# Kernel tuning notes

Hardware: AMD Instinct MI355X
Metric: run time of the kernel (lower is better)

The kernel has to match this reference:

```python
import jax, jax.numpy as jnp
import numpy as np

D_MODEL = 768; N_LAYERS = 4; SOC_WINDOW = 10
D_INNER = 2 * D_MODEL; D_STATE = 16; DT_RANK = D_MODEL // 16; D_CONV = 4
EPS = 1e-5
B, T = 4, 1024


def setup_inputs() -> dict:
    key = jax.random.key(0)
    ks = jax.random.split(key, 10)
    w = lambda k, s, sc=0.02: jax.random.normal(k, s, jnp.float32) * sc
    return {
        "x": jax.random.normal(ks[0], (B, T, 2 + SOC_WINDOW), jnp.float32),
        "inp_w": w(ks[1], (D_MODEL, 2 + SOC_WINDOW)),
        "inp_b": jnp.zeros((D_MODEL,), jnp.float32),
        "in_proj_w": w(ks[2], (N_LAYERS, 2 * D_INNER, D_MODEL)),
        "conv_w": w(ks[3], (N_LAYERS, D_INNER, D_CONV), 0.1),
        "conv_b": jnp.zeros((N_LAYERS, D_INNER), jnp.float32),
        "x_proj_w": w(ks[4], (N_LAYERS, DT_RANK + 2 * D_STATE, D_INNER)),
        "dt_proj_w": w(ks[5], (N_LAYERS, D_INNER, DT_RANK), 0.05),
        "dt_proj_b": w(ks[6], (N_LAYERS, D_INNER), 0.5),
        "A_log": jnp.tile(jnp.log(jnp.arange(1.0, D_STATE + 1.0, dtype=jnp.float32)), (N_LAYERS, D_INNER, 1)),
        "D_skip": jnp.ones((N_LAYERS, D_INNER), jnp.float32),
        "out_proj_w": w(ks[7], (N_LAYERS, D_MODEL, D_INNER)),
        "ln_w": jnp.ones((N_LAYERS, D_MODEL), jnp.float32),
        "norm_w": jnp.ones((D_MODEL,), jnp.float32),
        "head_w": w(ks[8], (1, D_MODEL)),
        "head_b": jnp.zeros((1,), jnp.float32),
    }


def _rmsnorm(x, w):
    return x * jax.lax.rsqrt(jnp.mean(x * x, axis=-1, keepdims=True) + EPS) * w


def _mamba_block(x, in_w, cw, cb, xp_w, dtw, dtb, A_log, Dsk, out_w):
    Bsz = x.shape[0]
    xz = jnp.einsum('btd,ed->bte', x, in_w)            # (B,T,2*D_INNER)
    xx, z = jnp.split(xz, 2, axis=-1)
    # causal depthwise conv1d (pad left d_conv-1, truncate to T)
    xc = jax.lax.conv_general_dilated(
        jnp.swapaxes(xx, 1, 2), cw[:, None, :], (1,), [(D_CONV - 1, 0)],
        feature_group_count=D_INNER, dimension_numbers=('NCH', 'OIH', 'NCH'))
    xx = jax.nn.silu(jnp.swapaxes(xc + cb[None, :, None], 1, 2))  # (B,T,D_INNER)
    dbc = jnp.einsum('btd,ed->bte', xx, xp_w)          # (B,T,dt_rank+2*N)
    delta = jax.nn.softplus(jnp.einsum('btr,dr->btd', dbc[..., :DT_RANK], dtw) + dtb)
    Bm = dbc[..., DT_RANK:DT_RANK + D_STATE]           # (B,T,N)
    Cm = dbc[..., DT_RANK + D_STATE:]                  # (B,T,N)
    A = -jnp.exp(A_log)                                # (D_INNER,N)

    def step(h, inp):
        d_t, x_t, b_t, c_t = inp                       # (B,Din),(B,Din),(B,N),(B,N)
        h = jnp.exp(d_t[..., None] * A) * h + (d_t * x_t)[..., None] * b_t[:, None, :]
        return h, jnp.einsum('bdn,bn->bd', h, c_t)

    h0 = jnp.zeros((Bsz, D_INNER, D_STATE), x.dtype)
    _, ys = jax.lax.scan(step, h0, (jnp.moveaxis(delta, 1, 0), jnp.moveaxis(xx, 1, 0),
                                    jnp.moveaxis(Bm, 1, 0), jnp.moveaxis(Cm, 1, 0)))
    y = jnp.moveaxis(ys, 0, 1) + Dsk * xx
    y = y * jax.nn.silu(z)
    return jnp.einsum('bte,de->btd', y, out_w)


def reference(x, inp_w, inp_b, in_proj_w, conv_w, conv_b, x_proj_w, dt_proj_w, dt_proj_b,
              A_log, D_skip, out_proj_w, ln_w, norm_w, head_w, head_b):
    h = jnp.einsum('btf,df->btd', x, inp_w) + inp_b
    for l in range(N_LAYERS):
        h = h + _mamba_block(_rmsnorm(h, ln_w[l]), in_proj_w[l], conv_w[l], conv_b[l],
                             x_proj_w[l], dt_proj_w[l], dt_proj_b[l], A_log[l],
                             D_skip[l], out_proj_w[l])
    h = _rmsnorm(h, norm_w)
    y = jnp.einsum('btd,od->bto', h, head_w) + head_b
    return y[..., 0]
```

## Files before the change

kernel.cpp:

```cpp
#include <hip/hip_runtime.h>
#include <stdint.h>

#define D_MODEL   768
#define D_INNER   1536
#define D_STATE   16
#define DT_RANK   48
#define NB        4
#define TSEQ      1024
#define NTOK      4096
#define EPS       1e-5f
#define CHUNK     32
#define NCHUNK    32
#define XP_N      128

typedef __bf16 bf16;
typedef __bf16 bf16x8 __attribute__((ext_vector_type(8)));
typedef float  floatx4 __attribute__((ext_vector_type(4)));

__device__ __forceinline__ float silu_f(float v)     { return v / (1.f + __expf(-v)); }
__device__ __forceinline__ float softplus_f(float v) { return v > 20.f ? v : __logf(1.f + __expf(v)); }

__device__ __forceinline__ void async_ld16(const void* g, void* l) {
  __builtin_amdgcn_global_load_lds((__attribute__((address_space(1))) uint32_t*)g,
                                   (__attribute__((address_space(3))) uint32_t*)l, 16, 0, 0);
}

__global__ __launch_bounds__(256) void prep_k(const float* __restrict__ win, const float* __restrict__ wout,
                                              bf16* __restrict__ bin, bf16* __restrict__ bout) {
  const int i = blockIdx.x * 256 + threadIdx.x;
  const int NIN = 4 * 3072 * 768;
  if (i < NIN) bin[i] = (bf16)win[i];
  else         bout[i - NIN] = (bf16)wout[i - NIN];
}

__global__ __launch_bounds__(256) void prep_xp_k(const float* __restrict__ w, bf16* __restrict__ wb) {
  const int i = blockIdx.x * 256 + threadIdx.x;
  const int k = i % 1536;
  const int r = (i / 1536) % XP_N;
  const int l = i / (1536 * XP_N);
  wb[i] = (r < 80) ? (bf16)w[((size_t)l * 80 + r) * 1536 + k] : (bf16)0.f;
}

__global__ __launch_bounds__(256) void input_proj_k(const float* __restrict__ x, const float* __restrict__ w,
                                                    const float* __restrict__ bvec, float* __restrict__ h) {
  const int idx = blockIdx.x * 256 + threadIdx.x;
  const int d = idx % D_MODEL;
  const int t = idx / D_MODEL;
  float acc = bvec[d];
  #pragma unroll
  for (int f = 0; f < 12; ++f) acc = fmaf(x[t * 12 + f], w[d * 12 + f], acc);
  h[idx] = acc;
}

__global__ __launch_bounds__(256) void rmsnorm_k(const float* __restrict__ h, const float* __restrict__ lnw,
                                                 bf16* __restrict__ xn) {
  const int t = blockIdx.x;
  const float* __restrict__ hr = h + (size_t)t * D_MODEL;
  float v[3];
  float ss = 0.f;
  #pragma unroll
  for (int i = 0; i < 3; ++i) { v[i] = hr[threadIdx.x + i * 256]; ss = fmaf(v[i], v[i], ss); }
  #pragma unroll
  for (int o = 32; o > 0; o >>= 1) ss += __shfl_down(ss, o, 64);
  __shared__ float red[4];
  if ((threadIdx.x & 63) == 0) red[threadIdx.x >> 6] = ss;
  __syncthreads();
  const float tot = red[0] + red[1] + red[2] + red[3];
  const float rs = rsqrtf(tot / (float)D_MODEL + EPS);
  #pragma unroll
  for (int i = 0; i < 3; ++i) {
    const int d = threadIdx.x + i * 256;
    xn[(size_t)t * D_MODEL + d] = (bf16)(v[i] * rs * lnw[d]);
  }
}

template <int MODE>
__global__ __launch_bounds__(256) void gemm_bt(const bf16* __restrict__ A, const bf16* __restrict__ B,
                                               float* __restrict__ C, const int N, const int K, const int kLen) {
  alignas(16) __shared__ bf16 As[128 * 32];
  alignas(16) __shared__ bf16 Bs[128 * 32];
  const int tid = threadIdx.x;
  const int lane = tid & 63;
  const int wid = tid >> 6;
  const int wm = wid & 1, wn = wid >> 1;
  const int m0 = blockIdx.x * 128, n0 = blockIdx.y * 128;
  const int kOff = blockIdx.z * kLen;

  floatx4 acc[4][4];
  #pragma unroll
  for (int i = 0; i < 4; ++i)
    #pragma unroll
    for (int j = 0; j < 4; ++j) acc[i][j] = (floatx4){0.f, 0.f, 0.f, 0.f};

  const int srow = lane >> 2;
  const int skp  = (lane & 3) * 8;
  const int fr = lane & 15;
  const int fk = (lane >> 4) * 8;

  for (int k0 = 0; k0 < kLen; k0 += 32) {
    __syncthreads();
    #pragma unroll
    for (int i = 0; i < 2; ++i) {
      const int seg = wid * 2 + i;
      const int row = seg * 16 + srow;
      async_ld16(A + (size_t)(m0 + row) * K + kOff + k0 + skp, (char*)As + seg * 1024);
      async_ld16(B + (size_t)(n0 + row) * K + kOff + k0 + skp, (char*)Bs + seg * 1024);
    }
    __syncthreads();
    bf16x8 a[4], b[4];
    #pragma unroll
    for (int t = 0; t < 4; ++t) {
      a[t] = *(const bf16x8*)&As[(wm * 64 + t * 16 + fr) * 32 + fk];
      b[t] = *(const bf16x8*)&Bs[(wn * 64 + t * 16 + fr) * 32 + fk];
    }
    #pragma unroll
    for (int i = 0; i < 4; ++i)
      #pragma unroll
      for (int j = 0; j < 4; ++j)
        acc[i][j] = __builtin_amdgcn_mfma_f32_16x16x32_bf16(a[i], b[j], acc[i][j], 0, 0, 0);
  }

  const int quad = lane >> 4, col = lane & 15;
  #pragma unroll
  for (int i = 0; i < 4; ++i)
    #pragma unroll
    for (int j = 0; j < 4; ++j) {
      const int gm0 = m0 + wm * 64 + i * 16 + quad * 4;
      const int gn  = n0 + wn * 64 + j * 16 + col;
      #pragma unroll
      for (int r = 0; r < 4; ++r) {
        const size_t off = (size_t)(gm0 + r) * N + gn;
        const float v = acc[i][j][r];
        if (MODE == 0) C[off] = v;
        else           atomicAdd(&C[off], v);
      }
    }
}

__global__ __launch_bounds__(256) void conv_silu_k(const float* __restrict__ xz, const float* __restrict__ cw,
                                                   const float* __restrict__ cb, float* __restrict__ xx,
                                                   bf16* __restrict__ xxb) {
  const int idx = blockIdx.x * 256 + threadIdx.x;
  const int d = idx % D_INNER;
  const int bt = idx / D_INNER;
  const int t = bt & (TSEQ - 1);
  float acc = cb[d];
  #pragma unroll
  for (int j = 0; j < 4; ++j) {
    const int tt = t - 3 + j;
    if (tt >= 0) acc = fmaf(xz[(size_t)(bt - 3 + j) * (2 * D_INNER) + d], cw[d * 4 + j], acc);
  }
  const float s = silu_f(acc);
  xx[idx] = s;
  xxb[idx] = (bf16)s;
}

__global__ __launch_bounds__(256) void dtproj_k(const float* __restrict__ dbc, const float* __restrict__ dtw,
                                                const float* __restrict__ dtb, float* __restrict__ delta) {
  const int d = blockIdx.y * 256 + threadIdx.x;
  const int t0 = blockIdx.x * 16;
  float w[DT_RANK];
  #pragma unroll
  for (int k = 0; k < DT_RANK; k += 4) {
    const float4 t4 = *(const float4*)&dtw[(size_t)d * DT_RANK + k];
    w[k] = t4.x; w[k + 1] = t4.y; w[k + 2] = t4.z; w[k + 3] = t4.w;
  }
  const float bias = dtb[d];
  for (int m = 0; m < 16; ++m) {
    const float* __restrict__ db = dbc + (size_t)(t0 + m) * XP_N;
    float acc = bias;
    #pragma unroll
    for (int k = 0; k < DT_RANK; ++k) acc = fmaf(db[k], w[k], acc);
    delta[(size_t)(t0 + m) * D_INNER + d] = softplus_f(acc);
  }
}

__global__ __launch_bounds__(256) void scan_p1_k(const float* __restrict__ delta, const float* __restrict__ xx,
                                                 const float* __restrict__ dbc, const float* __restrict__ Alog,
                                                 float* __restrict__ P, float* __restrict__ S) {
  const int c = blockIdx.x;
  const int d = blockIdx.y * 256 + threadIdx.x;
  const int b = blockIdx.z;
  float A[16], Sv[16], Pv[16];
  #pragma unroll
  for (int n = 0; n < 16; ++n) {
    A[n] = -__expf(Alog[(size_t)d * 16 + n]);
    Sv[n] = 0.f; Pv[n] = 1.f;
  }
  const int bt0 = b * TSEQ + c * CHUNK;
  for (int tt = 0; tt < CHUNK; ++tt) {
    const size_t bt = bt0 + tt;
    const float du  = delta[bt * D_INNER + d];
    const float xv  = xx[bt * D_INNER + d];
    const float dux = du * xv;
    const float* __restrict__ Bp = dbc + bt * XP_N + DT_RANK;
    #pragma unroll
    for (int n = 0; n < 16; ++n) {
      const float e = __expf(du * A[n]);
      Sv[n] = fmaf(e, Sv[n], dux * Bp[n]);
      Pv[n] *= e;
    }
  }
  const size_t base = ((size_t)(b * NCHUNK + c) * 16) * D_INNER + d;
  #pragma unroll
  for (int n = 0; n < 16; ++n) {
    P[base + (size_t)n * D_INNER] = Pv[n];
    S[base + (size_t)n * D_INNER] = Sv[n];
  }
}

__global__ __launch_bounds__(256) void scan_fold_k(const float* __restrict__ P, const float* __restrict__ S,
                                                   float* __restrict__ Hin) {
  const int idx = blockIdx.x * 256 + threadIdx.x;
  const int d = idx % D_INNER;
  const int bn = idx / D_INNER;
  const int n = bn & 15;
  const int b = bn >> 4;
  float H = 0.f;
  #pragma unroll 4
  for (int c = 0; c < NCHUNK; ++c) {
    const size_t off = ((size_t)((b * NCHUNK + c) * 16 + n)) * D_INNER + d;
    Hin[off] = H;
    H = fmaf(P[off], H, S[off]);
  }
}

__global__ __launch_bounds__(256) void scan_p3_k(const float* __restrict__ delta, const float* __restrict__ xx,
                                                 const float* __restrict__ dbc, const float* __restrict__ Alog,
                                                 const float* __restrict__ Hin,
                                                 const float* __restrict__ xz, const float* __restrict__ Dsk,
                                                 bf16* __restrict__ yg) {
  const int c = blockIdx.x;
  const int d = blockIdx.y * 256 + threadIdx.x;
  const int b = blockIdx.z;
  const size_t hbase = ((size_t)(b * NCHUNK + c) * 16) * D_INNER + d;
  float A[16], H[16];
  #pragma unroll
  for (int n = 0; n < 16; ++n) {
    A[n] = -__expf(Alog[(size_t)d * 16 + n]);
    H[n] = Hin[hbase + (size_t)n * D_INNER];
  }
  const float dsk = Dsk[d];
  const int bt0 = b * TSEQ + c * CHUNK;
  for (int tt = 0; tt < CHUNK; ++tt) {
    const size_t bt = bt0 + tt;
    const float du  = delta[bt * D_INNER + d];
    const float xv  = xx[bt * D_INNER + d];
    const float dux = du * xv;
    const float* __restrict__ Bp = dbc + bt * XP_N + DT_RANK;
    const float* __restrict__ Cp = Bp + 16;
    float y = 0.f;
    #pragma unroll
    for (int n = 0; n < 16; ++n) {
      const float e = __expf(du * A[n]);
      H[n] = fmaf(e, H[n], dux * Bp[n]);
      y = fmaf(H[n], Cp[n], y);
    }
    const float z = xz[bt * (2 * D_INNER) + D_INNER + d];
    yg[bt * D_INNER + d] = (bf16)((y + dsk * xv) * silu_f(z));
  }
}

__global__ __launch_bounds__(256) void final_k(const float* __restrict__ h, const float* __restrict__ nw,
                                               const float* __restrict__ hw, const float* __restrict__ hb,
                                               float* __restrict__ out) {
  const int t = blockIdx.x;
  const float* __restrict__ hr = h + (size_t)t * D_MODEL;
  float ss = 0.f, dt_ = 0.f;
  #pragma unroll
  for (int i = 0; i < 3; ++i) {
    const int d = threadIdx.x + i * 256;
    const float v = hr[d];
    ss  = fmaf(v, v, ss);
    dt_ = fmaf(v, nw[d] * hw[d], dt_);
  }
  #pragma unroll
  for (int o = 32; o > 0; o >>= 1) { ss += __shfl_down(ss, o, 64); dt_ += __shfl_down(dt_, o, 64); }
  __shared__ float r0[4], r1[4];
  if ((threadIdx.x & 63) == 0) { r0[threadIdx.x >> 6] = ss; r1[threadIdx.x >> 6] = dt_; }
  __syncthreads();
  if (threadIdx.x == 0) {
    const float sst = r0[0] + r0[1] + r0[2] + r0[3];
    const float dtt = r1[0] + r1[1] + r1[2] + r1[3];
    out[t] = dtt * rsqrtf(sst / (float)D_MODEL + EPS) + hb[0];
  }
}

extern "C" void kernel_launch(void* const* d_in, const int* in_sizes, int n_in,
                              void* d_out, int out_size, void* d_ws, size_t ws_size,
                              hipStream_t stream) {
  (void)in_sizes; (void)n_in; (void)out_size; (void)ws_size;
  const float* x     = (const float*)d_in[0];
  const float* inpw  = (const float*)d_in[1];
  const float* inpb  = (const float*)d_in[2];
  const float* inprj = (const float*)d_in[3];
  const float* convw = (const float*)d_in[4];
  const float* convb = (const float*)d_in[5];
  const float* xprjw = (const float*)d_in[6];
  const float* dtw   = (const float*)d_in[7];
  const float* dtb   = (const float*)d_in[8];
  const float* alog  = (const float*)d_in[9];
  const float* dskip = (const float*)d_in[10];
  const float* outw  = (const float*)d_in[11];
  const float* lnw   = (const float*)d_in[12];
  const float* normw = (const float*)d_in[13];
  const float* headw = (const float*)d_in[14];
  const float* headb = (const float*)d_in[15];
  float* out = (float*)d_out;

  char* p = (char*)d_ws;
  auto take = [&](size_t bytes) { char* q = p; p += (bytes + 255) & ~(size_t)255; return q; };
  bf16*  wbin  = (bf16*) take((size_t)4 * 3072 * 768 * 2);
  bf16*  wbout = (bf16*) take((size_t)4 * 768 * 1536 * 2);
  bf16*  wbxp  = (bf16*) take((size_t)4 * XP_N * 1536 * 2);
  float* h     = (float*)take((size_t)NTOK * D_MODEL * 4);
  bf16*  xn    = (bf16*) take((size_t)NTOK * D_MODEL * 2);
  float* xz    = (float*)take((size_t)NTOK * 2 * D_INNER * 4);
  float* xxa   = (float*)take((size_t)NTOK * D_INNER * 4);
  bf16*  xxb   = (bf16*) take((size_t)NTOK * D_INNER * 2);
  float* dbc   = (float*)take((size_t)NTOK * XP_N * 4);
  float* dlt   = (float*)take((size_t)NTOK * D_INNER * 4);
  float* Pb    = (float*)take((size_t)NB * NCHUNK * 16 * D_INNER * 4);
  float* Sb    = (float*)take((size_t)NB * NCHUNK * 16 * D_INNER * 4);
  float* Hin   = (float*)take((size_t)NB * NCHUNK * 16 * D_INNER * 4);
  bf16*  yg    = (bf16*) take((size_t)NTOK * D_INNER * 2);

  prep_k<<<55296, 256, 0, stream>>>(inprj, outw, wbin, wbout);
  prep_xp_k<<<4 * XP_N * 1536 / 256, 256, 0, stream>>>(xprjw, wbxp);
  input_proj_k<<<NTOK * D_MODEL / 256, 256, 0, stream>>>(x, inpw, inpb, h);

  for (int l = 0; l < 4; ++l) {
    rmsnorm_k<<<NTOK, 256, 0, stream>>>(h, lnw + l * D_MODEL, xn);
    gemm_bt<0><<<dim3(32, 24, 1), 256, 0, stream>>>(xn, wbin + (size_t)l * 3072 * 768, xz, 3072, 768, 768);
    conv_silu_k<<<NTOK * D_INNER / 256, 256, 0, stream>>>(xz, convw + l * D_INNER * 4, convb + l * D_INNER,
                                                          xxa, xxb);
    hipMemsetAsync(dbc, 0, (size_t)NTOK * XP_N * 4, stream);
    gemm_bt<2><<<dim3(32, 1, 4), 256, 0, stream>>>(xxb, wbxp + (size_t)l * XP_N * 1536, dbc, XP_N, 1536, 384);
    dtproj_k<<<dim3(NTOK / 16, 6), 256, 0, stream>>>(dbc, dtw + (size_t)l * D_INNER * DT_RANK,
                                                     dtb + l * D_INNER, dlt);
    scan_p1_k<<<dim3(NCHUNK, 6, NB), 256, 0, stream>>>(dlt, xxa, dbc, alog + (size_t)l * D_INNER * 16, Pb, Sb);
    scan_fold_k<<<NB * 16 * D_INNER / 256, 256, 0, stream>>>(Pb, Sb, Hin);
    scan_p3_k<<<dim3(NCHUNK, 6, NB), 256, 0, stream>>>(dlt, xxa, dbc, alog + (size_t)l * D_INNER * 16,
                                                       Hin, xz, dskip + l * D_INNER, yg);
    gemm_bt<2><<<dim3(32, 6, 2), 256, 0, stream>>>(yg, wbout + (size_t)l * 768 * 1536, h, 768, 1536, 768);
  }

  final_k<<<NTOK, 256, 0, stream>>>(h, normw, headw, headb, out);
}
```

Measured before the change: 986.3 us.

## Fuse dt projection into scan passes and store xz/xx activations in bf16

Removes the standalone dtproj kernel and the delta buffer; both scan passes now recompute delta from dbc with a 48-wide dot product and softplus per timestep. The in_proj GEMM writes bf16 instead of fp32, the fp32 copy of the conv output is dropped so the scans read bf16 xx, and the fold writes carry-in states in place into S. This cuts global memory traffic, at the cost of doing the dt projection twice and lower precision for the x/z activations.

```diff
diff --git a/kernel.cpp b/kernel.cpp
--- a/kernel.cpp
+++ b/kernel.cpp
@@ -76,7 +76,7 @@
 
 template <int MODE>
 __global__ __launch_bounds__(256) void gemm_bt(const bf16* __restrict__ A, const bf16* __restrict__ B,
-                                               float* __restrict__ C, const int N, const int K, const int kLen) {
+                                               void* __restrict__ Cv, const int N, const int K, const int kLen) {
   alignas(16) __shared__ bf16 As[128 * 32];
   alignas(16) __shared__ bf16 Bs[128 * 32];
   const int tid = threadIdx.x;
@@ -131,15 +131,15 @@
       for (int r = 0; r < 4; ++r) {
         const size_t off = (size_t)(gm0 + r) * N + gn;
         const float v = acc[i][j][r];
-        if (MODE == 0) C[off] = v;
-        else           atomicAdd(&C[off], v);
+        if (MODE == 0)      ((float*)Cv)[off] = v;
+        else if (MODE == 1) ((bf16*)Cv)[off] = (bf16)v;
+        else                atomicAdd(&((float*)Cv)[off], v);
       }
     }
 }
 
-__global__ __launch_bounds__(256) void conv_silu_k(const float* __restrict__ xz, const float* __restrict__ cw,
-                                                   const float* __restrict__ cb, float* __restrict__ xx,
-                                                   bf16* __restrict__ xxb) {
+__global__ __launch_bounds__(256) void conv_silu_k(const bf16* __restrict__ xz, const float* __restrict__ cw,
+                                                   const float* __restrict__ cb, bf16* __restrict__ xxb) {
   const int idx = blockIdx.x * 256 + threadIdx.x;
   const int d = idx % D_INNER;
   const int bt = idx / D_INNER;
@@ -148,39 +148,25 @@
   #pragma unroll
   for (int j = 0; j < 4; ++j) {
     const int tt = t - 3 + j;
-    if (tt >= 0) acc = fmaf(xz[(size_t)(bt - 3 + j) * (2 * D_INNER) + d], cw[d * 4 + j], acc);
-  }
-  const float s = silu_f(acc);
-  xx[idx] = s;
-  xxb[idx] = (bf16)s;
-}
-
-__global__ __launch_bounds__(256) void dtproj_k(const float* __restrict__ dbc, const float* __restrict__ dtw,
-                                                const float* __restrict__ dtb, float* __restrict__ delta) {
-  const int d = blockIdx.y * 256 + threadIdx.x;
-  const int t0 = blockIdx.x * 16;
-  float w[DT_RANK];
-  #pragma unroll
-  for (int k = 0; k < DT_RANK; k += 4) {
-    const float4 t4 = *(const float4*)&dtw[(size_t)d * DT_RANK + k];
-    w[k] = t4.x; w[k + 1] = t4.y; w[k + 2] = t4.z; w[k + 3] = t4.w;
-  }
-  const float bias = dtb[d];
-  for (int m = 0; m < 16; ++m) {
-    const float* __restrict__ db = dbc + (size_t)(t0 + m) * XP_N;
-    float acc = bias;
-    #pragma unroll
-    for (int k = 0; k < DT_RANK; ++k) acc = fmaf(db[k], w[k], acc);
-    delta[(size_t)(t0 + m) * D_INNER + d] = softplus_f(acc);
-  }
-}
-
-__global__ __launch_bounds__(256) void scan_p1_k(const float* __restrict__ delta, const float* __restrict__ xx,
-                                                 const float* __restrict__ dbc, const float* __restrict__ Alog,
+    if (tt >= 0) acc = fmaf((float)xz[(size_t)(bt - 3 + j) * (2 * D_INNER) + d], cw[d * 4 + j], acc);
+  }
+  xxb[idx] = (bf16)silu_f(acc);
+}
+
+__global__ __launch_bounds__(256) void scan_p1_k(const bf16* __restrict__ xxb, const float* __restrict__ dbc,
+                                                 const float* __restrict__ dtw, const float* __restrict__ dtb,
+                                                 const float* __restrict__ Alog,
                                                  float* __restrict__ P, float* __restrict__ S) {
   const int c = blockIdx.x;
   const int d = blockIdx.y * 256 + threadIdx.x;
   const int b = blockIdx.z;
+  float w[DT_RANK];
+  #pragma unroll
+  for (int k = 0; k < DT_RANK; k += 4) {
+    const float4 t4 = *(const float4*)&dtw[(size_t)d * DT_RANK + k];
+    w[k] = t4.x; w[k + 1] = t4.y; w[k + 2] = t4.z; w[k + 3] = t4.w;
+  }
+  const float bias = dtb[d];
   float A[16], Sv[16], Pv[16];
   #pragma unroll
   for (int n = 0; n < 16; ++n) {
@@ -190,10 +176,14 @@
   const int bt0 = b * TSEQ + c * CHUNK;
   for (int tt = 0; tt < CHUNK; ++tt) {
     const size_t bt = bt0 + tt;
-    const float du  = delta[bt * D_INNER + d];
-    const float xv  = xx[bt * D_INNER + d];
+    const float* __restrict__ db = dbc + bt * XP_N;
+    float dacc = bias;
+    #pragma unroll
+    for (int k = 0; k < DT_RANK; ++k) dacc = fmaf(db[k], w[k], dacc);
+    const float du  = softplus_f(dacc);
+    const float xv  = (float)xxb[bt * D_INNER + d];
     const float dux = du * xv;
-    const float* __restrict__ Bp = dbc + bt * XP_N + DT_RANK;
+    const float* __restrict__ Bp = db + DT_RANK;
     #pragma unroll
     for (int n = 0; n < 16; ++n) {
       const float e = __expf(du * A[n]);
@@ -209,8 +199,7 @@
   }
 }
 
-__global__ __launch_bounds__(256) void scan_fold_k(const float* __restrict__ P, const float* __restrict__ S,
-                                                   float* __restrict__ Hin) {
+__global__ __launch_bounds__(256) void scan_fold_k(const float* __restrict__ P, float* __restrict__ S) {
   const int idx = blockIdx.x * 256 + threadIdx.x;
   const int d = idx % D_INNER;
   const int bn = idx / D_INNER;
@@ -220,19 +209,28 @@
   #pragma unroll 4
   for (int c = 0; c < NCHUNK; ++c) {
     const size_t off = ((size_t)((b * NCHUNK + c) * 16 + n)) * D_INNER + d;
-    Hin[off] = H;
-    H = fmaf(P[off], H, S[off]);
-  }
-}
-
-__global__ __launch_bounds__(256) void scan_p3_k(const float* __restrict__ delta, const float* __restrict__ xx,
-                                                 const float* __restrict__ dbc, const float* __restrict__ Alog,
+    const float Pv = P[off], Sv = S[off];
+    S[off] = H;
+    H = fmaf(Pv, H, Sv);
+  }
+}
+
+__global__ __launch_bounds__(256) void scan_p3_k(const bf16* __restrict__ xxb, const float* __restrict__ dbc,
+                                                 const float* __restrict__ dtw, const float* __restrict__ dtb,
+                                                 const float* __restrict__ Alog,
                                                  const float* __restrict__ Hin,
-                                                 const float* __restrict__ xz, const float* __restrict__ Dsk,
+                                                 const bf16* __restrict__ xz, const float* __restrict__ Dsk,
                                                  bf16* __restrict__ yg) {
   const int c = blockIdx.x;
   const int d = blockIdx.y * 256 + threadIdx.x;
   const int b = blockIdx.z;
+  float w[DT_RANK];
+  #pragma unroll
+  for (int k = 0; k < DT_RANK; k += 4) {
+    const float4 t4 = *(const float4*)&dtw[(size_t)d * DT_RANK + k];
+    w[k] = t4.x; w[k + 1] = t4.y; w[k + 2] = t4.z; w[k + 3] = t4.w;
+  }
+  const float bias = dtb[d];
   const size_t hbase = ((size_t)(b * NCHUNK + c) * 16) * D_INNER + d;
   float A[16], H[16];
   #pragma unroll
@@ -244,11 +242,15 @@
   const int bt0 = b * TSEQ + c * CHUNK;
   for (int tt = 0; tt < CHUNK; ++tt) {
     const size_t bt = bt0 + tt;
-    const float du  = delta[bt * D_INNER + d];
-    const float xv  = xx[bt * D_INNER + d];
+    const float* __restrict__ db = dbc + bt * XP_N;
+    float dacc = bias;
+    #pragma unroll
+    for (int k = 0; k < DT_RANK; ++k) dacc = fmaf(db[k], w[k], dacc);
+    const float du  = softplus_f(dacc);
+    const float xv  = (float)xxb[bt * D_INNER + d];
     const float dux = du * xv;
-    const float* __restrict__ Bp = dbc + bt * XP_N + DT_RANK;
-    const float* __restrict__ Cp = Bp + 16;
+    const float* __restrict__ Bp = db + DT_RANK;
+    const float* __restrict__ Cp = db + DT_RANK + 16;
     float y = 0.f;
     #pragma unroll
     for (int n = 0; n < 16; ++n) {
@@ -256,7 +258,7 @@
       H[n] = fmaf(e, H[n], dux * Bp[n]);
       y = fmaf(H[n], Cp[n], y);
     }
-    const float z = xz[bt * (2 * D_INNER) + D_INNER + d];
+    const float z = (float)xz[bt * (2 * D_INNER) + D_INNER + d];
     yg[bt * D_INNER + d] = (bf16)((y + dsk * xv) * silu_f(z));
   }
 }
@@ -315,14 +317,11 @@
   bf16*  wbxp  = (bf16*) take((size_t)4 * XP_N * 1536 * 2);
   float* h     = (float*)take((size_t)NTOK * D_MODEL * 4);
   bf16*  xn    = (bf16*) take((size_t)NTOK * D_MODEL * 2);
-  float* xz    = (float*)take((size_t)NTOK * 2 * D_INNER * 4);
-  float* xxa   = (float*)take((size_t)NTOK * D_INNER * 4);
+  bf16*  xzb   = (bf16*) take((size_t)NTOK * 2 * D_INNER * 2);
   bf16*  xxb   = (bf16*) take((size_t)NTOK * D_INNER * 2);
   float* dbc   = (float*)take((size_t)NTOK * XP_N * 4);
-  float* dlt   = (float*)take((size_t)NTOK * D_INNER * 4);
   float* Pb    = (float*)take((size_t)NB * NCHUNK * 16 * D_INNER * 4);
   float* Sb    = (float*)take((size_t)NB * NCHUNK * 16 * D_INNER * 4);
-  float* Hin   = (float*)take((size_t)NB * NCHUNK * 16 * D_INNER * 4);
   bf16*  yg    = (bf16*) take((size_t)NTOK * D_INNER * 2);
 
   prep_k<<<55296, 256, 0, stream>>>(inprj, outw, wbin, wbout);
@@ -331,17 +330,16 @@
 
   for (int l = 0; l < 4; ++l) {
     rmsnorm_k<<<NTOK, 256, 0, stream>>>(h, lnw + l * D_MODEL, xn);
-    gemm_bt<0><<<dim3(32, 24, 1), 256, 0, stream>>>(xn, wbin + (size_t)l * 3072 * 768, xz, 3072, 768, 768);
-    conv_silu_k<<<NTOK * D_INNER / 256, 256, 0, stream>>>(xz, convw + l * D_INNER * 4, convb + l * D_INNER,
-                                                          xxa, xxb);
+    gemm_bt<1><<<dim3(32, 24, 1), 256, 0, stream>>>(xn, wbin + (size_t)l * 3072 * 768, xzb, 3072, 768, 768);
+    conv_silu_k<<<NTOK * D_INNER / 256, 256, 0, stream>>>(xzb, convw + l * D_INNER * 4, convb + l * D_INNER, xxb);
     hipMemsetAsync(dbc, 0, (size_t)NTOK * XP_N * 4, stream);
     gemm_bt<2><<<dim3(32, 1, 4), 256, 0, stream>>>(xxb, wbxp + (size_t)l * XP_N * 1536, dbc, XP_N, 1536, 384);
-    dtproj_k<<<dim3(NTOK / 16, 6), 256, 0, stream>>>(dbc, dtw + (size_t)l * D_INNER * DT_RANK,
-                                                     dtb + l * D_INNER, dlt);
-    scan_p1_k<<<dim3(NCHUNK, 6, NB), 256, 0, stream>>>(dlt, xxa, dbc, alog + (size_t)l * D_INNER * 16, Pb, Sb);
-    scan_fold_k<<<NB * 16 * D_INNER / 256, 256, 0, stream>>>(Pb, Sb, Hin);
-    scan_p3_k<<<dim3(NCHUNK, 6, NB), 256, 0, stream>>>(dlt, xxa, dbc, alog + (size_t)l * D_INNER * 16,
-                                                       Hin, xz, dskip + l * D_INNER, yg);
+    scan_p1_k<<<dim3(NCHUNK, 6, NB), 256, 0, stream>>>(xxb, dbc, dtw + (size_t)l * D_INNER * DT_RANK,
+                                                       dtb + l * D_INNER, alog + (size_t)l * D_INNER * 16, Pb, Sb);
+    scan_fold_k<<<NB * 16 * D_INNER / 256, 256, 0, stream>>>(Pb, Sb);
+    scan_p3_k<<<dim3(NCHUNK, 6, NB), 256, 0, stream>>>(xxb, dbc, dtw + (size_t)l * D_INNER * DT_RANK,
+                                                       dtb + l * D_INNER, alog + (size_t)l * D_INNER * 16,
+                                                       Sb, xzb, dskip + l * D_INNER, yg);
     gemm_bt<2><<<dim3(32, 6, 2), 256, 0, stream>>>(yg, wbout + (size_t)l * 768 * 1536, h, 768, 1536, 768);
   }
 
```

Measured after the change: 968.9 us. Within noise of the previous version (-1.8%).
